# Kernel optimization log

Measured on AMD Instinct MI355X. Metric: run time of the kernel, lower is better.

## Reference

```python
import jax, jax.numpy as jnp
import numpy as np


def _nearest_down(x, oh, ow):
    # torch F.interpolate(mode='nearest'): src_idx = floor(dst_idx * in/out)
    ih, iw = x.shape[-2], x.shape[-1]
    hi = jnp.floor(jnp.arange(oh) * (ih / oh)).astype(jnp.int32)
    wi = jnp.floor(jnp.arange(ow) * (iw / ow)).astype(jnp.int32)
    return x[..., hi, :][..., :, wi]


def setup_inputs() -> dict:
    key = jax.random.key(0)
    k1, k2, k3, k4 = jax.random.split(key, 4)
    B, Cf, Hf, Wf = 8, 256, 128, 128   # encoder feature map (stride 4)
    HL, WL = 512, 512                  # label / logit resolution
    C_OLD, NUM_CLASSES = 16, 21
    return {
        "outputs": jnp.zeros((1,), jnp.float32),        # overwritten in original forward
        "outputs_old": jax.random.normal(k1, (B, C_OLD, HL, WL), jnp.float32),
        "features": jax.random.normal(k2, (B, Cf, Hf, Wf), jnp.float32),
        "features_old": jnp.zeros((1,), jnp.float32),   # unused by this branch
        "labels": jax.random.randint(k3, (B, HL, WL), 0, NUM_CLASSES),
        "prototypes": jax.random.normal(k4, (NUM_CLASSES, Cf), jnp.float32),
        "classes_old": 16,
        "incremental_step": 1,
    }


def reference(outputs, outputs_old, features, features_old, labels, prototypes,
              classes_old, incremental_step):
    # Default branch: val=False, sequential=False, loss_de_prototypes_sumafter=False.
    if incremental_step == 0:
        return jnp.asarray(0.0, jnp.float32)
    B, C, H, W = features.shape
    # downsample labels to feature resolution (nearest)
    labels_down = _nearest_down(labels[:, None, :, :], H, W)      # [B,1,H,W] int
    bgr_mask = labels_down == 0
    # old-model pseudo-labels, masked to background of current labels
    pred_old = jnp.argmax(outputs_old, axis=1, keepdims=True)      # [B,1,HL,WL]
    pred_old_down = _nearest_down(pred_old, H, W)                  # [B,1,H,W]
    pseudo = jnp.where(bgr_mask, pred_old_down, 0)                 # [B,1,H,W]

    ids = pseudo.reshape(-1)                                       # [N]
    feats = jnp.transpose(features, (0, 2, 3, 1)).reshape(-1, C)   # [N,C]
    proto = jax.lax.stop_gradient(prototypes)                      # .detach()

    # per-pixel MSE (mean over channels) vs the prototype of its pseudo-class
    per_pix = jnp.mean(jnp.square(feats - proto[ids]), axis=-1)    # [N]

    sums = jax.ops.segment_sum(per_pix, ids, num_segments=classes_old)
    counts = jax.ops.segment_sum(jnp.ones_like(per_pix), ids, num_segments=classes_old)
    # mean over pixels of each present class; absent classes contribute 0
    per_class = jnp.where(counts > 0, sums / jnp.maximum(counts, 1.0), 0.0)
    # class 0 is excluded (cl_present drops background)
    return jnp.sum(per_class[1:])
```

## Files before the change

kernel.cpp:

```cpp
#include <hip/hip_runtime.h>

#define BB   8
#define CF   256
#define HF   128
#define WF   128
#define HL   512
#define WL   512
#define COLD 16


__global__ __launch_bounds__(256) void proto_loss_sparse(
    const float* __restrict__ outputs_old,
    const float* __restrict__ features,
    const int*   __restrict__ labels,
    const float* __restrict__ prototypes,
    float* __restrict__ ws)
{
    __shared__ int   plist[WF];
    __shared__ float ssum[16];
    __shared__ int   scnt[16];
    __shared__ int   lcnt;

    const int t   = threadIdx.x;
    const int blk = blockIdx.x;
    const int b   = blk >> 7;
    const int h   = blk & (HF - 1);

    if (t < 16) { ssum[t] = 0.0f; scnt[t] = 0; }
    if (t == 0) lcnt = 0;
    __syncthreads();

    if (t < WF) {
        const int w   = t;
        const int lab = labels[(b * HL + h * 4) * WL + w * 4];
        if (lab == 0) {
            const float* po = outputs_old
                + ((size_t)(b * COLD) * HL + (size_t)(h * 4)) * WL + w * 4;
            float best = po[0];
            int   id   = 0;
            #pragma unroll
            for (int c = 1; c < COLD; ++c) {
                float v = po[(size_t)c * (HL * WL)];
                if (v > best) { best = v; id = c; }
            }
            if (id > 0) {
                int pos = atomicAdd(&lcnt, 1);
                plist[pos] = w | (id << 16);
                atomicAdd(&scnt[id], 1);
            }
        }
    }
    __syncthreads();
    const int m = lcnt;

    const int wave = t >> 6;
    const int lane = t & 63;
    for (int p = wave; p < m; p += 4) {
        const int e  = plist[p];
        const int w  = e & 0xffff;
        const int id = e >> 16;
        const float* fb = features + ((size_t)(b * CF) * HF + h) * WF + w;
        const float* pr = prototypes + id * CF;
        float acc = 0.0f;
        #pragma unroll
        for (int k = 0; k < 4; ++k) {
            const int c = lane + 64 * k;
            const float d = fb[(size_t)c * (HF * WF)] - pr[c];
            acc += d * d;
        }
        #pragma unroll
        for (int off = 32; off > 0; off >>= 1)
            acc += __shfl_xor(acc, off, 64);
        if (lane == 0)
            atomicAdd(&ssum[id], acc * (1.0f / CF));
    }
    __syncthreads();

    if (t < 16) {
        ws[blk * 32 + t]      = ssum[t];
        ws[blk * 32 + 16 + t] = (float)scnt[t];
    }
}

__global__ __launch_bounds__(256) void proto_loss_final(
    const float* __restrict__ ws,
    const int*   __restrict__ classes_old,
    const int*   __restrict__ inc_step,
    float* __restrict__ out)
{
    __shared__ float red[8 * 32];
    const int t   = threadIdx.x;
    const int s   = t & 31;
    const int grp = t >> 5;
    float acc = 0.0f;
    for (int i = grp; i < BB * HF; i += 8)
        acc += ws[i * 32 + s];
    red[grp * 32 + s] = acc;
    __syncthreads();
    if (t == 0) {
        float r = 0.0f;
        if (*inc_step != 0) {
            int K = *classes_old;
            if (K > 16) K = 16;
            for (int id = 1; id < K; ++id) {
                float sum = 0.0f, cnt = 0.0f;
                for (int g = 0; g < 8; ++g) {
                    sum += red[g * 32 + id];
                    cnt += red[g * 32 + 16 + id];
                }
                if (cnt > 0.0f) r += sum / cnt;
            }
        }
        out[0] = r;
    }
}

extern "C" void kernel_launch(void* const* d_in, const int* in_sizes, int n_in,
                              void* d_out, int out_size, void* d_ws, size_t ws_size,
                              hipStream_t stream)
{
    const float* outputs_old = (const float*)d_in[1];
    const float* features    = (const float*)d_in[2];
    const int*   labels      = (const int*)d_in[4];
    const float* prototypes  = (const float*)d_in[5];
    const int*   classes_old = (const int*)d_in[6];
    const int*   inc_step    = (const int*)d_in[7];

    float* ws = (float*)d_ws;

    proto_loss_sparse<<<dim3(BB * HF), dim3(256), 0, stream>>>(
        outputs_old, features, labels, prototypes, ws);
    proto_loss_final<<<dim3(1), dim3(256), 0, stream>>>(
        ws, classes_old, inc_step, (float*)d_out);
}
```

Measured before the change: 291.7 us.

## Replace sparse per-pixel wave reduction with coalesced float4 channel-tiled accumulation

Splits each feature row across two blocks of 64 pixels. Feature loads are reorganised so each thread reads a float4 of four adjacent pixels for 16 channels, with partials reduced through shared memory. This replaces the compacted pixel list, where each wave handled one pixel with strided scalar loads. The aim is better-coalesced feature reads and twice as many blocks. The trade-off is that feature data is now loaded for every 4-pixel group that has any non-zero id, rather than only for the selected pixels.

```diff
diff --git a/kernel.cpp b/kernel.cpp
--- a/kernel.cpp
+++ b/kernel.cpp
@@ -7,72 +7,85 @@
 #define HL   512
 #define WL   512
 #define COLD 16
+#define WPB  64
+#define NBLK (BB * HF * 2)
 
 
-__global__ __launch_bounds__(256) void proto_loss_sparse(
+__global__ __launch_bounds__(256) void proto_loss_main(
     const float* __restrict__ outputs_old,
     const float* __restrict__ features,
     const int*   __restrict__ labels,
     const float* __restrict__ prototypes,
     float* __restrict__ ws)
 {
-    __shared__ int   plist[WF];
+    __shared__ int   sids[WPB];
+    __shared__ float spartial[16][WPB];
     __shared__ float ssum[16];
     __shared__ int   scnt[16];
-    __shared__ int   lcnt;
 
-    const int t   = threadIdx.x;
-    const int blk = blockIdx.x;
-    const int b   = blk >> 7;
-    const int h   = blk & (HF - 1);
+    const int t    = threadIdx.x;
+    const int blk  = blockIdx.x;
+    const int row  = blk >> 1;
+    const int b    = row >> 7;
+    const int h    = row & (HF - 1);
+    const int w0   = (blk & 1) * WPB;
 
     if (t < 16) { ssum[t] = 0.0f; scnt[t] = 0; }
-    if (t == 0) lcnt = 0;
-    __syncthreads();
 
-    if (t < WF) {
-        const int w   = t;
+    if (t < WPB) {
+        const int w   = w0 + t;
+        int id = 0;
         const int lab = labels[(b * HL + h * 4) * WL + w * 4];
         if (lab == 0) {
             const float* po = outputs_old
                 + ((size_t)(b * COLD) * HL + (size_t)(h * 4)) * WL + w * 4;
             float best = po[0];
-            int   id   = 0;
             #pragma unroll
             for (int c = 1; c < COLD; ++c) {
                 float v = po[(size_t)c * (HL * WL)];
                 if (v > best) { best = v; id = c; }
             }
-            if (id > 0) {
-                int pos = atomicAdd(&lcnt, 1);
-                plist[pos] = w | (id << 16);
-                atomicAdd(&scnt[id], 1);
-            }
+        }
+        sids[t] = id;
+    }
+    __syncthreads();
+
+    const int w4    = (t & 15) * 4;
+    const int c_off = t >> 4;
+    const int id0 = sids[w4 + 0];
+    const int id1 = sids[w4 + 1];
+    const int id2 = sids[w4 + 2];
+    const int id3 = sids[w4 + 3];
+
+    float a0 = 0.f, a1 = 0.f, a2 = 0.f, a3 = 0.f;
+    if ((id0 | id1 | id2 | id3) != 0) {
+        const float* pr0 = prototypes + id0 * CF;
+        const float* pr1 = prototypes + id1 * CF;
+        const float* pr2 = prototypes + id2 * CF;
+        const float* pr3 = prototypes + id3 * CF;
+        const float* fb  = features + ((size_t)(b * CF) * HF + h) * WF + w0 + w4;
+        #pragma unroll 4
+        for (int k = 0; k < 16; ++k) {
+            const int c = k * 16 + c_off;
+            const float4 f = *(const float4*)(fb + (size_t)c * (HF * WF));
+            float d0 = f.x - pr0[c]; a0 += d0 * d0;
+            float d1 = f.y - pr1[c]; a1 += d1 * d1;
+            float d2 = f.z - pr2[c]; a2 += d2 * d2;
+            float d3 = f.w - pr3[c]; a3 += d3 * d3;
         }
     }
+    *(float4*)&spartial[c_off][w4] = make_float4(a0, a1, a2, a3);
     __syncthreads();
-    const int m = lcnt;
 
-    const int wave = t >> 6;
-    const int lane = t & 63;
-    for (int p = wave; p < m; p += 4) {
-        const int e  = plist[p];
-        const int w  = e & 0xffff;
-        const int id = e >> 16;
-        const float* fb = features + ((size_t)(b * CF) * HF + h) * WF + w;
-        const float* pr = prototypes + id * CF;
-        float acc = 0.0f;
-        #pragma unroll
-        for (int k = 0; k < 4; ++k) {
-            const int c = lane + 64 * k;
-            const float d = fb[(size_t)c * (HF * WF)] - pr[c];
-            acc += d * d;
+    if (t < WPB) {
+        const int id = sids[t];
+        if (id > 0) {
+            float pp = 0.f;
+            #pragma unroll
+            for (int g = 0; g < 16; ++g) pp += spartial[g][t];
+            atomicAdd(&ssum[id], pp * (1.0f / CF));
+            atomicAdd(&scnt[id], 1);
         }
-        #pragma unroll
-        for (int off = 32; off > 0; off >>= 1)
-            acc += __shfl_xor(acc, off, 64);
-        if (lane == 0)
-            atomicAdd(&ssum[id], acc * (1.0f / CF));
     }
     __syncthreads();
 
@@ -93,7 +106,7 @@
     const int s   = t & 31;
     const int grp = t >> 5;
     float acc = 0.0f;
-    for (int i = grp; i < BB * HF; i += 8)
+    for (int i = grp; i < NBLK; i += 8)
         acc += ws[i * 32 + s];
     red[grp * 32 + s] = acc;
     __syncthreads();
@@ -128,7 +141,7 @@
 
     float* ws = (float*)d_ws;
 
-    proto_loss_sparse<<<dim3(BB * HF), dim3(256), 0, stream>>>(
+    proto_loss_main<<<dim3(NBLK), dim3(256), 0, stream>>>(
         outputs_old, features, labels, prototypes, ws);
     proto_loss_final<<<dim3(1), dim3(256), 0, stream>>>(
         ws, classes_old, inc_step, (float*)d_out);
```

Measured after the change: 326.0 us. +11.7%, slower.
